# Performance work log

Hardware: AMD Instinct MI355X
Metric: run time of the kernel (lower is better)

The kernel has to match this reference:

```python
import jax, jax.numpy as jnp
import numpy as np

N = 8192        # nodes
V = 50000       # vocab = len(dict_node_names)
EMB = 256       # embedding_dim
XI = EMB // 2   # x_increased_dim = 128
DIN = EMB + XI  # 384, SelfAtt_ dim
H = 4           # n_heads
D = 128         # WGAT output_dim per head (fusion dim)
E = 131072      # edges
CHUNK = 32768   # chunk_size (E % CHUNK == 0)


def _ln(x, g, b, eps=1e-5):
    m = jnp.mean(x, axis=-1, keepdims=True)
    v = jnp.mean((x - m) ** 2, axis=-1, keepdims=True)
    return (x - m) * jax.lax.rsqrt(v + eps) * g + b


def _wgat(emb, src, dst, edge_attr, wi, bi, wj, bj, wt, bt, attn):
    # x_i = features at destination (aggregation target), x_j = source/neighbor
    x_i = emb[dst]                                   # [E, din]
    x_j = emb[src]                                   # [E, din]
    h = (x_i @ wi + bi).reshape(E, H, D) + (x_j @ wj + bj).reshape(E, H, D)
    a = jnp.einsum('ehd,hd->eh', h, attn)            # [E, H]
    a = a * edge_attr[:, None]                       # edge weights pre-softmax
    # faithful chunked softmax: normalize over edges WITHIN each chunk (dim=0 per chunk)
    a = jax.nn.softmax(a.reshape(E // CHUNK, CHUNK, H), axis=1).reshape(E, H)
    xt = (x_j @ wt + bt).reshape(E, H, D)            # [E, H, D]
    msg = jnp.einsum('ehd,eh->ed', xt, a)            # sum over heads -> [E, D]
    return jax.ops.segment_sum(msg, dst, num_segments=N)  # aggr='add'


def _emb_forward(ids, edge_index, x, edge_attr, embed,
                 qkv_w, qkv_b, proj_w, proj_b, fuse_w, fuse_b, ln1_g, ln1_b,
                 wi0, bi0, wj0, bj0, wt0, bt0, attn0, skip0_w, skip0_b,
                 wi1, bi1, wj1, bj1, wt1, bt1, attn1, skip1_w, skip1_b,
                 ln2_g, ln2_b):
    E_i = embed[ids]                                 # [N, EMB] gather
    z = jnp.concatenate([jnp.tile(x, (1, XI)), E_i], axis=-1)   # [N, DIN]
    # SelfAtt_ : full N x N attention over nodes, scale = DIN**-0.5
    qkv = z @ qkv_w + qkv_b
    q, k, v = jnp.split(qkv, 3, axis=-1)
    att = jax.nn.softmax((q @ k.T) * (DIN ** -0.5), axis=-1) @ v
    z = att @ proj_w + proj_b                        # [N, DIN]
    emb = jax.nn.silu(_ln(z @ fuse_w + fuse_b, ln1_g, ln1_b)) + E_i  # [N, EMB]
    src, dst = edge_index[0], edge_index[1]
    emb = _wgat(emb, src, dst, edge_attr, wi0, bi0, wj0, bj0, wt0, bt0, attn0)  # [N, D]
    s0 = emb @ skip0_w + skip0_b
    emb = _wgat(emb, src, dst, edge_attr, wi1, bi1, wj1, bj1, wt1, bt1, attn1)  # [N, D]
    s1 = emb @ skip1_w + skip1_b
    emb = _ln(emb + (s0 + s1) * 0.5, ln2_g, ln2_b)
    return emb


def setup_inputs() -> dict:
    key = jax.random.key(0)
    ks = jax.random.split(key, 32)

    def w(k, shape, scale=0.05):
        return jax.random.normal(k, shape, jnp.float32) * scale

    inp = {}
    inp['ids'] = jax.random.randint(ks[0], (N,), 0, V)
    inp['x'] = jax.random.normal(ks[1], (N, 1), jnp.float32)
    inp['edge_attr'] = jax.random.uniform(ks[2], (E,), jnp.float32)
    inp['edge_index'] = jax.random.randint(ks[3], (2, E), 0, N)
    inp['embed'] = w(ks[4], (V, EMB), 1.0)
    inp['qkv_w'] = w(ks[5], (DIN, 3 * DIN)); inp['qkv_b'] = jnp.zeros((3 * DIN,), jnp.float32)
    inp['proj_w'] = w(ks[6], (DIN, DIN));    inp['proj_b'] = jnp.zeros((DIN,), jnp.float32)
    inp['fuse_w'] = w(ks[7], (DIN, EMB));    inp['fuse_b'] = jnp.zeros((EMB,), jnp.float32)
    inp['ln1_g'] = jnp.ones((EMB,), jnp.float32); inp['ln1_b'] = jnp.zeros((EMB,), jnp.float32)
    # WGAT layer 0: in=EMB, out=D per head, H heads
    inp['wi0'] = w(ks[8], (EMB, H * D));  inp['bi0'] = jnp.zeros((H * D,), jnp.float32)
    inp['wj0'] = w(ks[9], (EMB, H * D));  inp['bj0'] = jnp.zeros((H * D,), jnp.float32)
    inp['wt0'] = w(ks[10], (EMB, H * D)); inp['bt0'] = jnp.zeros((H * D,), jnp.float32)
    inp['attn0'] = w(ks[11], (H, D), 0.1)
    inp['skip0_w'] = w(ks[12], (D, D));   inp['skip0_b'] = jnp.zeros((D,), jnp.float32)
    # WGAT layer 1: in=D
    inp['wi1'] = w(ks[13], (D, H * D));   inp['bi1'] = jnp.zeros((H * D,), jnp.float32)
    inp['wj1'] = w(ks[14], (D, H * D));   inp['bj1'] = jnp.zeros((H * D,), jnp.float32)
    inp['wt1'] = w(ks[15], (D, H * D));   inp['bt1'] = jnp.zeros((H * D,), jnp.float32)
    inp['attn1'] = w(ks[16], (H, D), 0.1)
    inp['skip1_w'] = w(ks[17], (D, D));   inp['skip1_b'] = jnp.zeros((D,), jnp.float32)
    inp['ln2_g'] = jnp.ones((D,), jnp.float32); inp['ln2_b'] = jnp.zeros((D,), jnp.float32)
    return inp


def reference(ids, x, edge_attr, edge_index, embed,
              qkv_w, qkv_b, proj_w, proj_b, fuse_w, fuse_b, ln1_g, ln1_b,
              wi0, bi0, wj0, bj0, wt0, bt0, attn0, skip0_w, skip0_b,
              wi1, bi1, wj1, bj1, wt1, bt1, attn1, skip1_w, skip1_b,
              ln2_g, ln2_b):
    emb = _emb_forward(ids, edge_index, x, edge_attr, embed,
                       qkv_w, qkv_b, proj_w, proj_b, fuse_w, fuse_b, ln1_g, ln1_b,
                       wi0, bi0, wj0, bj0, wt0, bt0, attn0, skip0_w, skip0_b,
                       wi1, bi1, wj1, bj1, wt1, bt1, attn1, skip1_w, skip1_b,
                       ln2_g, ln2_b)
    return (emb, embed, ids)
```

## Files before the change

### kernel.cpp

```cpp
#include <hip/hip_runtime.h>

typedef __attribute__((ext_vector_type(8))) short bfrag;
typedef __attribute__((ext_vector_type(4))) float f4;

#define MFMA(a,b,c) __builtin_amdgcn_mfma_f32_16x16x32_bf16(a,b,c,0,0,0)

__device__ __forceinline__ unsigned short f2b(float x){
  union { float f; unsigned int u; } v; v.f = x;
  unsigned int r = v.u + 0x7fffu + ((v.u >> 16) & 1u);
  return (unsigned short)(r >> 16);
}
__device__ __forceinline__ float b2f(unsigned short h){
  union { unsigned int u; float f; } v; v.u = ((unsigned int)h) << 16;
  return v.f;
}

__global__ __launch_bounds__(256) void k_prep(
    const float* __restrict__ qkv_w, const float* __restrict__ proj_w,
    const float* __restrict__ proj_b, const float* __restrict__ fuse_w,
    const float* __restrict__ fuse_b,
    const float* __restrict__ wt0,
    const float* __restrict__ wt1, const float* __restrict__ sk0w,
    const float* __restrict__ wi0, const float* __restrict__ bi0,
    const float* __restrict__ wj0, const float* __restrict__ bj0,
    const float* __restrict__ wi1, const float* __restrict__ bi1,
    const float* __restrict__ wj1, const float* __restrict__ bj1,
    const float* __restrict__ attn0, const float* __restrict__ attn1,
    const float* __restrict__ bt0, const float* __restrict__ bt1,
    const float* __restrict__ sk0b,
    const float* __restrict__ embed, const int* __restrict__ ids,
    unsigned short* __restrict__ BtQKV, unsigned short* __restrict__ BtW2,
    unsigned short* __restrict__ BtT0, unsigned short* __restrict__ BtT1,
    float* __restrict__ biasW2,
    float* __restrict__ biasT0, float* __restrict__ biasT1,
    float* __restrict__ wsum, float* __restrict__ Ei,
    float* __restrict__ out)
{
  int b = blockIdx.x, t = threadIdx.x;
  if (b < 1152) {
    int idx = b*256 + t; int k = idx/1152, n = idx - k*1152;
    BtQKV[(size_t)n*256 + k] = f2b(qkv_w[128*1152 + idx]);
  } else if (b < 1536) {
    int k = b - 1152;
    float s = 0.f;
    for (int j = 0; j < 384; ++j) s += proj_w[(size_t)k*384 + j] * fuse_w[(size_t)j*256 + t];
    BtW2[(size_t)t*384 + k] = f2b(s);
  } else if (b == 1536) {
    float s = fuse_b[t];
    for (int j = 0; j < 384; ++j) s += proj_b[j] * fuse_w[(size_t)j*256 + t];
    biasW2[t] = s;
  } else if (b < 2049) {
    int idx = (b-1537)*256 + t; int k = idx/512, n = idx - k*512;
    BtT0[(size_t)n*256 + k] = f2b(wt0[idx]);
  } else if (b < 2305) {
    int idx = (b-2049)*256 + t; int k = idx/512, n = idx - k*512;
    BtT1[(size_t)n*128 + k] = f2b(wt1[idx]);
  } else if (b < 2369) {
    int idx = (b-2305)*256 + t; int k = idx/128, n = idx - k*128;
    BtT1[(size_t)(520+n)*128 + k] = f2b(sk0w[idx]);
  } else if (b < 2373) {
    int idx = (b-2369)*256 + t;
    int h = idx >> 8, k = idx & 255;
    float s = 0.f;
    for (int d = 0; d < 128; ++d) s += wi0[(size_t)k*512 + h*128 + d] * attn0[h*128 + d];
    BtT0[(size_t)(512 + h)*256 + k] = f2b(s);
    if (idx < 4) {
      float sb = 0.f;
      for (int d = 0; d < 128; ++d) sb += bi0[idx*128 + d] * attn0[idx*128 + d];
      biasT0[512 + idx] = sb;
    }
  } else if (b < 2377) {
    int idx = (b-2373)*256 + t;
    int h = idx >> 8, k = idx & 255;
    float s = 0.f;
    for (int d = 0; d < 128; ++d) s += wj0[(size_t)k*512 + h*128 + d] * attn0[h*128 + d];
    BtT0[(size_t)(516 + h)*256 + k] = f2b(s);
    if (idx < 4) {
      float sb = 0.f;
      for (int d = 0; d < 128; ++d) sb += bj0[idx*128 + d] * attn0[idx*128 + d];
      biasT0[516 + idx] = sb;
    }
  } else if (b < 2379) {
    int idx = (b-2377)*256 + t;
    int h = idx >> 7, k = idx & 127;
    float s = 0.f;
    for (int d = 0; d < 128; ++d) s += wi1[(size_t)k*512 + h*128 + d] * attn1[h*128 + d];
    BtT1[(size_t)(512 + h)*128 + k] = f2b(s);
    if (idx < 4) {
      float sb = 0.f;
      for (int d = 0; d < 128; ++d) sb += bi1[idx*128 + d] * attn1[idx*128 + d];
      biasT1[512 + idx] = sb;
    }
  } else if (b < 2381) {
    int idx = (b-2379)*256 + t;
    int h = idx >> 7, k = idx & 127;
    float s = 0.f;
    for (int d = 0; d < 128; ++d) s += wj1[(size_t)k*512 + h*128 + d] * attn1[h*128 + d];
    BtT1[(size_t)(516 + h)*128 + k] = f2b(s);
    if (idx < 4) {
      float sb = 0.f;
      for (int d = 0; d < 128; ++d) sb += bj1[idx*128 + d] * attn1[idx*128 + d];
      biasT1[516 + idx] = sb;
    }
  } else if (b < 2383) {
    int idx = (b-2381)*256 + t; biasT0[idx] = bt0[idx];
  } else if (b < 2385) {
    int idx = (b-2383)*256 + t; biasT1[idx] = bt1[idx];
  } else if (b == 2385) {
    if (t < 128) biasT1[520 + t] = sk0b[t];
  } else if (b < 2391) {
    int n = (b-2386)*256 + t;
    if (n < 1152) {
      float s = 0.f;
      for (int k = 0; k < 128; ++k) s += qkv_w[(size_t)k*1152 + n];
      wsum[n] = s;
    }
  } else if (b < 4439) {
    int idx = (b-2391)*256 + t;
    int n = idx >> 6, c4 = idx & 63;
    reinterpret_cast<float4*>(Ei)[idx] =
        reinterpret_cast<const float4*>(embed + (size_t)ids[n]*256)[c4];
  } else {
    int i = (b-4439)*256 + t;
    if (i < 3200000)
      reinterpret_cast<float4*>(out)[262144 + i] = reinterpret_cast<const float4*>(embed)[i];
    if (i < 8192) out[13848576 + i] = (float)ids[i];
  }
}

__global__ void k_deg(const int* __restrict__ ei, int* __restrict__ deg){
  int e = blockIdx.x*256 + threadIdx.x; if (e >= 131072) return;
  atomicAdd(&deg[ei[131072 + e]], 1);
}

__global__ __launch_bounds__(1024) void k_scan(const int* __restrict__ deg,
                                               int* __restrict__ off, int* __restrict__ cursor){
  int t = threadIdx.x;
  int v[8]; int s = 0;
  #pragma unroll
  for (int i=0;i<8;++i){ v[i] = s; s += deg[t*8 + i]; }
  int lane = t & 63, w = t >> 6;
  int si = s;
  for (int o=1;o<64;o<<=1){ int u = __shfl_up(si, o); if (lane >= o) si += u; }
  __shared__ int wsum[16];
  if (lane == 63) wsum[w] = si;
  __syncthreads();
  if (t < 16) {
    int x = wsum[t];
    for (int o=1;o<16;o<<=1){ int u = __shfl_up(x, o); if (t >= o) x += u; }
    wsum[t] = x;
  }
  __syncthreads();
  int wbase = (w == 0) ? 0 : wsum[w-1];
  int base = wbase + (si - s);
  #pragma unroll
  for (int i=0;i<8;++i){ int o2 = base + v[i]; off[t*8+i] = o2; cursor[t*8+i] = o2; }
  if (t == 1023) off[8192] = wbase + si;
}

__global__ void k_fill(const int* __restrict__ ei, int* __restrict__ cursor,
                       int* __restrict__ elist){
  int e = blockIdx.x*256 + threadIdx.x; if (e >= 131072) return;
  int d = ei[131072 + e];
  int slot = atomicAdd(&cursor[d], 1);
  elist[slot] = e;
}

__global__ __launch_bounds__(256) void k_gemm(
    const float* __restrict__ A, int lda,
    const unsigned short* __restrict__ Bt, int K,
    const float* __restrict__ bias,
    float* __restrict__ C, int ldc, int mode,
    const float* __restrict__ xv, const float* __restrict__ wsum,
    unsigned short* __restrict__ qO, unsigned short* __restrict__ kO,
    unsigned short* __restrict__ vO,
    const unsigned short* __restrict__ opA, const float* __restrict__ cw,
    float* __restrict__ aux, int ncols)
{
  __shared__ unsigned short As[128*40];
  __shared__ unsigned short Bs[128*40];
  const int t = threadIdx.x;
  const int wid = t >> 6, l = t & 63;
  const int lr = l & 15, lg = l >> 4;
  const int arow0 = blockIdx.y*128, bn0 = blockIdx.x*128;
  const int wr = (wid >> 1)*64, wc = (wid & 1)*64;
  f4 zero = {0.f,0.f,0.f,0.f};
  f4 acc[4][4];
  #pragma unroll
  for (int i=0;i<4;++i)
    #pragma unroll
    for (int j=0;j<4;++j) acc[i][j] = zero;

  for (int k0 = 0; k0 < K; k0 += 32) {
    #pragma unroll
    for (int p=0;p<4;++p) {
      int row = p*32 + (t>>3);
      int c4  = (t&7)*4;
      ushort4 h4;
      if (mode == 2) {
        const float* w4 = &cw[(arow0+row)*4];
        float a0=0.f,a1=0.f,a2=0.f,a3=0.f;
        #pragma unroll
        for (int s=0;s<4;++s) {
          ushort4 u = *reinterpret_cast<const ushort4*>(
              opA + (size_t)s*3145728 + (size_t)(arow0+row)*384 + k0 + c4);
          float wv = w4[s];
          a0 += b2f(u.x)*wv; a1 += b2f(u.y)*wv; a2 += b2f(u.z)*wv; a3 += b2f(u.w)*wv;
        }
        h4.x = f2b(a0); h4.y = f2b(a1); h4.z = f2b(a2); h4.w = f2b(a3);
      } else {
        float4 v = *reinterpret_cast<const float4*>(A + (size_t)(arow0+row)*lda + k0 + c4);
        h4.x = f2b(v.x); h4.y = f2b(v.y); h4.z = f2b(v.z); h4.w = f2b(v.w);
      }
      *reinterpret_cast<ushort4*>(&As[row*40 + c4]) = h4;
    }
    #pragma unroll
    for (int p=0;p<2;++p) {
      int n  = p*64 + (t>>2);
      int c8 = (t&3)*8;
      int4 v = *reinterpret_cast<const int4*>(Bt + (size_t)(bn0+n)*K + k0 + c8);
      *reinterpret_cast<int4*>(&Bs[n*40 + c8]) = v;
    }
    __syncthreads();
    bfrag af[4], bfm[4];
    #pragma unroll
    for (int mi=0;mi<4;++mi) af[mi] = *reinterpret_cast<const bfrag*>(&As[(wr+mi*16+lr)*40 + lg*8]);
    #pragma unroll
    for (int ni=0;ni<4;++ni) bfm[ni] = *reinterpret_cast<const bfrag*>(&Bs[(wc+ni*16+lr)*40 + lg*8]);
    #pragma unroll
    for (int mi=0;mi<4;++mi)
      #pragma unroll
      for (int ni=0;ni<4;++ni)
        acc[mi][ni] = MFMA(af[mi], bfm[ni], acc[mi][ni]);
    __syncthreads();
  }
  #pragma unroll
  for (int mi=0;mi<4;++mi) {
    #pragma unroll
    for (int ni=0;ni<4;++ni) {
      int col = bn0 + wc + ni*16 + lr;
      float bv = bias[col];
      float wsv = (mode==1) ? wsum[col] : 0.f;
      #pragma unroll
      for (int i=0;i<4;++i) {
        int row = arow0 + wr + mi*16 + lg*4 + i;
        float val = acc[mi][ni][i] + bv;
        if (mode == 1) {
          val += xv[row]*wsv;
          if (col < 384) val *= 0.05103103631f;
          unsigned short hv = f2b(val);
          if (col < 384)      qO[(size_t)row*384 + col] = hv;
          else if (col < 768) kO[(size_t)row*384 + col - 384] = hv;
          else {
            int d = col - 768, j = row;
            size_t vidx = (size_t)(j >> 5)*12288 + (size_t)(d >> 4)*512
                        + (size_t)(d & 15)*32 + (size_t)((j & 31) >> 3)*8 + (j & 7);
            vO[vidx] = hv;
          }
        } else if (mode == 3) {
          if (col < 512)      qO[(size_t)row*512 + col] = f2b(val);
          else if (col < 520) C[(size_t)row*8 + col - 512] = val;
          else if (col < ncols) aux[(size_t)row*128 + col - 520] = val;
        } else {
          C[(size_t)row*ldc + col] = val;
        }
      }
    }
  }
}

__global__ __launch_bounds__(256,2) void k_flash(
    const unsigned short* __restrict__ qg,
    const unsigned short* __restrict__ kg,
    const unsigned short* __restrict__ vg,
    unsigned short* __restrict__ Opart, float* __restrict__ mpart, float* __restrict__ lpart)
{
  __shared__ unsigned short Ks[32*384];
  __shared__ unsigned short Ps[64*40];
  __shared__ float f_s[64];

  const int t = threadIdx.x;
  const int w = t >> 6, l = t & 63;
  const int lr = l & 15, lg = l >> 4;
  const int qbi = blockIdx.x >> 2, split = blockIdx.x & 3;
  const int qbase = qbi * 64;

  #define STAGE_K(JJ) do { \
    _Pragma("unroll") \
    for (int p_=0;p_<6;++p_) { \
      int idx_ = p_*256 + t; \
      int row_ = idx_ / 48, uu_ = idx_ - row_*48; \
      int ug_ = uu_ ^ (row_ & 7); \
      const unsigned short* gp_ = kg + (size_t)((JJ) + row_)*384 + ug_*8; \
      __builtin_amdgcn_global_load_lds((const __attribute__((address_space(1))) void*)gp_, \
          (__attribute__((address_space(3))) void*)&Ks[idx_*8], 16, 0, 0); \
    } } while(0)

  bfrag qf[12];
  #pragma unroll
  for (int kk=0;kk<12;++kk)
    qf[kk] = *reinterpret_cast<const bfrag*>(qg + (size_t)(qbase + w*16 + lr)*384 + kk*32 + lg*8);

  f4 zero = {0.f,0.f,0.f,0.f};
  f4 o[4][6];
  #pragma unroll
  for (int a=0;a<4;++a)
    #pragma unroll
    for (int b=0;b<6;++b) o[a][b] = zero;

  float m = -3e38f, lsum = 0.f;
  const int j0beg = split*2048, jend = j0beg + 2048;

  STAGE_K(j0beg);
  __syncthreads();

  for (int j0 = j0beg; j0 < jend; j0 += 32) {
    f4 s0 = zero, s1 = zero;
    __builtin_amdgcn_s_setprio(1);
    #pragma unroll
    for (int kk=0;kk<12;++kk) {
      int su = ((kk*4 + lg) ^ (lr & 7)) * 8;
      bfrag k0 = *reinterpret_cast<const bfrag*>(&Ks[lr*384 + su]);
      bfrag k1 = *reinterpret_cast<const bfrag*>(&Ks[(16+lr)*384 + su]);
      s0 = MFMA(k0, qf[kk], s0);
      s1 = MFMA(k1, qf[kk], s1);
    }
    __builtin_amdgcn_s_setprio(0);

    float mt = fmaxf(fmaxf(fmaxf(s0[0],s0[1]),fmaxf(s0[2],s0[3])),
                     fmaxf(fmaxf(s1[0],s1[1]),fmaxf(s1[2],s1[3])));
    mt = fmaxf(mt, __shfl_xor(mt,16));
    mt = fmaxf(mt, __shfl_xor(mt,32));
    bool grew = mt > m + 8.f;
    bool doresc = __any(grew);
    float mn = doresc ? fmaxf(m, mt) : m;
    float p0[4], p1[4];
    float sum = 0.f;
    #pragma unroll
    for (int i=0;i<4;++i) {
      p0[i] = __expf(s0[i]-mn); p1[i] = __expf(s1[i]-mn);
      sum += p0[i] + p1[i];
    }
    sum += __shfl_xor(sum,16);
    sum += __shfl_xor(sum,32);
    float f = 1.f;
    if (doresc) {
      f = __expf(m - mn);
      lsum = lsum * f + sum;
      m = mn;
    } else {
      lsum += sum;
    }

    unsigned int pk0 = (unsigned int)f2b(p0[0]) | ((unsigned int)f2b(p0[1]) << 16);
    unsigned int pk1 = (unsigned int)f2b(p0[2]) | ((unsigned int)f2b(p0[3]) << 16);
    unsigned int pk2 = (unsigned int)f2b(p1[0]) | ((unsigned int)f2b(p1[1]) << 16);
    unsigned int pk3 = (unsigned int)f2b(p1[2]) | ((unsigned int)f2b(p1[3]) << 16);
    int prow = (w*16 + lr)*40;
    *reinterpret_cast<unsigned int*>(&Ps[prow + lg*4])          = pk0;
    *reinterpret_cast<unsigned int*>(&Ps[prow + lg*4 + 2])      = pk1;
    *reinterpret_cast<unsigned int*>(&Ps[prow + 16 + lg*4])     = pk2;
    *reinterpret_cast<unsigned int*>(&Ps[prow + 16 + lg*4 + 2]) = pk3;
    if (lg == 0) f_s[w*16 + lr] = f;

    __syncthreads();

    if (j0 + 32 < jend) STAGE_K(j0 + 32);

    const int jt = j0 >> 5;
    bfrag vf[6];
    #pragma unroll
    for (int dt=0;dt<6;++dt)
      vf[dt] = *reinterpret_cast<const bfrag*>(
          vg + (size_t)jt*12288 + (size_t)(w*6 + dt)*512 + lr*32 + lg*8);

    bfrag pf[4];
    #pragma unroll
    for (int qt=0;qt<4;++qt)
      pf[qt] = *reinterpret_cast<const bfrag*>(&Ps[(qt*16+lr)*40 + lg*8]);
    #pragma unroll
    for (int qt=0;qt<4;++qt) {
      #pragma unroll
      for (int i=0;i<4;++i) {
        float frv = f_s[qt*16 + lg*4 + i];
        #pragma unroll
        for (int dt=0;dt<6;++dt) o[qt][dt][i] *= frv;
      }
    }
    __builtin_amdgcn_s_setprio(1);
    #pragma unroll
    for (int qt=0;qt<4;++qt)
      #pragma unroll
      for (int dt=0;dt<6;++dt)
        o[qt][dt] = MFMA(pf[qt], vf[dt], o[qt][dt]);
    __builtin_amdgcn_s_setprio(0);

    __syncthreads();
  }
  #undef STAGE_K

  unsigned short* Op = Opart + (size_t)split*8192*384;
  #pragma unroll
  for (int qt=0;qt<4;++qt)
    #pragma unroll
    for (int dt=0;dt<6;++dt)
      #pragma unroll
      for (int i=0;i<4;++i)
        Op[(size_t)(qbase + qt*16 + lg*4 + i)*384 + w*96 + dt*16 + lr] = f2b(o[qt][dt][i]);
  if (lg == 0) {
    mpart[split*8192 + qbase + w*16 + lr] = m;
    lpart[split*8192 + qbase + w*16 + lr] = lsum;
  }
}

__global__ void k_cw(const float* __restrict__ mp, const float* __restrict__ lp,
                     float* __restrict__ cw)
{
  int r = blockIdx.x*256 + threadIdx.x;
  float m0 = mp[r], m1 = mp[8192+r], m2 = mp[16384+r], m3 = mp[24576+r];
  float M = fmaxf(fmaxf(m0,m1), fmaxf(m2,m3));
  float w0 = __expf(m0-M), w1 = __expf(m1-M), w2 = __expf(m2-M), w3 = __expf(m3-M);
  float L = lp[r]*w0 + lp[8192+r]*w1 + lp[16384+r]*w2 + lp[24576+r]*w3;
  float inv = 1.f / L;
  float4 o4 = make_float4(w0*inv, w1*inv, w2*inv, w3*inv);
  *reinterpret_cast<float4*>(&cw[r*4]) = o4;
}

__global__ __launch_bounds__(256) void k_ln1(const float* __restrict__ pre, const float* __restrict__ Ei,
                      const float* __restrict__ g, const float* __restrict__ b,
                      float* __restrict__ out)
{
  int row = blockIdx.x, c = threadIdx.x;
  float v = pre[(size_t)row*256 + c];
  float s1 = v, s2 = v*v;
  #pragma unroll
  for (int o1=32;o1;o1>>=1){ s1 += __shfl_down(s1,o1); s2 += __shfl_down(s2,o1); }
  __shared__ float a1[4], a2[4];
  if ((c&63)==0){ a1[c>>6] = s1; a2[c>>6] = s2; }
  __syncthreads();
  float S1 = a1[0]+a1[1]+a1[2]+a1[3], S2 = a2[0]+a2[1]+a2[2]+a2[3];
  float mean = S1*(1.f/256.f), var = S2*(1.f/256.f) - mean*mean;
  float y = (v-mean)*rsqrtf(var+1e-5f)*g[c] + b[c];
  float sig = 1.f/(1.f+__expf(-y));
  out[(size_t)row*256 + c] = y*sig + Ei[(size_t)row*256 + c];
}

__global__ __launch_bounds__(256) void k_escore(const int* __restrict__ ei, const float* __restrict__ ea,
                         const float* __restrict__ SC, float* __restrict__ sc,
                         float* __restrict__ pm, float* __restrict__ ps)
{
  int e = blockIdx.x*256 + threadIdx.x;
  int s = ei[e], d = ei[131072 + e];
  float wv = ea[e];
  float4 ai = *reinterpret_cast<const float4*>(&SC[(size_t)d*8]);
  float4 aj = *reinterpret_cast<const float4*>(&SC[(size_t)s*8 + 4]);
  float4 o4 = make_float4((ai.x+aj.x)*wv, (ai.y+aj.y)*wv, (ai.z+aj.z)*wv, (ai.w+aj.w)*wv);
  *reinterpret_cast<float4*>(&sc[e*4]) = o4;

  float sv[4] = {o4.x, o4.y, o4.z, o4.w};
  __shared__ float sm_[4][4], ss_[4][4];
  int lane = threadIdx.x & 63, wvid = threadIdx.x >> 6;
  #pragma unroll
  for (int h=0; h<4; ++h) {
    float m = sv[h], s2 = 1.f;
    #pragma unroll
    for (int o1=32;o1;o1>>=1) {
      float om = __shfl_xor(m,o1), os = __shfl_xor(s2,o1);
      float M2 = fmaxf(m,om);
      s2 = s2*__expf(m-M2) + os*__expf(om-M2);
      m = M2;
    }
    if (lane==0){ sm_[wvid][h]=m; ss_[wvid][h]=s2; }
  }
  __syncthreads();
  if (threadIdx.x < 4) {
    int h = threadIdx.x;
    float M = sm_[0][h], S = ss_[0][h];
    #pragma unroll
    for (int i=1;i<4;++i){
      float M2 = fmaxf(M, sm_[i][h]);
      S = S*__expf(M-M2) + ss_[i][h]*__expf(sm_[i][h]-M2);
      M = M2;
    }
    pm[blockIdx.x*4+h] = M; ps[blockIdx.x*4+h] = S;
  }
}

__global__ __launch_bounds__(128) void k_cfin(const float* __restrict__ pm, const float* __restrict__ ps,
                                              float* __restrict__ mx, float* __restrict__ sm)
{
  int ch = blockIdx.x;
  int c = ch >> 2, h = ch & 3;
  int t = threadIdx.x;
  float M = pm[(c*128 + t)*4 + h], S = ps[(c*128 + t)*4 + h];
  int lane = t & 63;
  #pragma unroll
  for (int o1=32;o1;o1>>=1){
    float om = __shfl_xor(M,o1), os = __shfl_xor(S,o1);
    float M2 = fmaxf(M,om);
    S = S*__expf(M-M2) + os*__expf(om-M2);
    M = M2;
  }
  __shared__ float am[2], as[2];
  if (lane==0){ am[t>>6]=M; as[t>>6]=S; }
  __syncthreads();
  if (t==0){
    float M2 = fmaxf(am[0],am[1]);
    float Sf = as[0]*__expf(am[0]-M2) + as[1]*__expf(am[1]-M2);
    mx[ch]=M2; sm[ch]=Sf;
  }
}

__global__ void k_pnorm(float* __restrict__ sc, const float* __restrict__ mx,
                        const float* __restrict__ sm)
{
  int i = blockIdx.x*256 + threadIdx.x;
  int e = i >> 2, h = i & 3;
  int ch = (e >> 15)*4 + h;
  sc[i] = __expf(sc[i] - mx[ch]) / sm[ch];
}

__global__ __launch_bounds__(128) void k_aggr(const int* __restrict__ off,
                      const int* __restrict__ elist, const int* __restrict__ ei,
                      const float* __restrict__ sc,
                      const unsigned short* __restrict__ Tb, float* __restrict__ g)
{
  int n = blockIdx.x, d = threadIdx.x;
  int qb = off[n], qe = off[n+1];
  float acc = 0.f;
  for (int q = qb; q < qe; ++q) {
    int e = elist[q];
    int s = ei[e];
    float4 p = *reinterpret_cast<const float4*>(&sc[e*4]);
    const unsigned short* Tr = Tb + (size_t)s*512;
    acc += p.x*b2f(Tr[d]) + p.y*b2f(Tr[128+d]) + p.z*b2f(Tr[256+d]) + p.w*b2f(Tr[384+d]);
  }
  g[(size_t)n*128 + d] = acc;
}

__global__ __launch_bounds__(128) void k_final(const float* __restrict__ g1, const float* __restrict__ aux,
                       const float* __restrict__ sw, const float* __restrict__ sb,
                       const float* __restrict__ lg2, const float* __restrict__ lb2,
                       float* __restrict__ out)
{
  int row = blockIdx.x, c = threadIdx.x;
  __shared__ float gr[128];
  float gv = g1[(size_t)row*128 + c];
  gr[c] = gv; __syncthreads();
  float s1 = sb[c];
  #pragma unroll 8
  for (int k=0;k<128;++k) s1 += gr[k]*sw[k*128 + c];
  float s0 = aux[(size_t)row*128 + c];
  float v = gv + 0.5f*(s0 + s1);
  float m1 = v, m2 = v*v;
  #pragma unroll
  for (int o1=32;o1;o1>>=1){ m1 += __shfl_down(m1,o1); m2 += __shfl_down(m2,o1); }
  __shared__ float a1[2], a2[2];
  if ((c&63)==0){ a1[c>>6]=m1; a2[c>>6]=m2; }
  __syncthreads();
  float S1 = a1[0]+a1[1], S2 = a2[0]+a2[1];
  float mean = S1*(1.f/128.f), var = S2*(1.f/128.f) - mean*mean;
  out[(size_t)row*128 + c] = (v-mean)*rsqrtf(var+1e-5f)*lg2[c] + lb2[c];
}

extern "C" void kernel_launch(void* const* d_in, const int* in_sizes, int n_in,
                              void* d_out, int out_size, void* d_ws, size_t ws_size,
                              hipStream_t stream)
{
  const int*   ids    = (const int*)  d_in[0];
  const float* x      = (const float*)d_in[1];
  const float* ea     = (const float*)d_in[2];
  const int*   eidx   = (const int*)  d_in[3];
  const float* embed  = (const float*)d_in[4];
  const float* qkv_w  = (const float*)d_in[5];
  const float* qkv_b  = (const float*)d_in[6];
  const float* proj_w = (const float*)d_in[7];
  const float* proj_b = (const float*)d_in[8];
  const float* fuse_w = (const float*)d_in[9];
  const float* fuse_b = (const float*)d_in[10];
  const float* ln1_g  = (const float*)d_in[11];
  const float* ln1_b  = (const float*)d_in[12];
  const float* wi0 = (const float*)d_in[13]; const float* bi0 = (const float*)d_in[14];
  const float* wj0 = (const float*)d_in[15]; const float* bj0 = (const float*)d_in[16];
  const float* wt0 = (const float*)d_in[17]; const float* bt0 = (const float*)d_in[18];
  const float* attn0 = (const float*)d_in[19];
  const float* sk0w = (const float*)d_in[20]; const float* sk0b = (const float*)d_in[21];
  const float* wi1 = (const float*)d_in[22]; const float* bi1 = (const float*)d_in[23];
  const float* wj1 = (const float*)d_in[24]; const float* bj1 = (const float*)d_in[25];
  const float* wt1 = (const float*)d_in[26]; const float* bt1 = (const float*)d_in[27];
  const float* attn1 = (const float*)d_in[28];
  const float* sk1w = (const float*)d_in[29]; const float* sk1b = (const float*)d_in[30];
  const float* ln2_g = (const float*)d_in[31]; const float* ln2_b = (const float*)d_in[32];

  char* ws = (char*)d_ws;
  const size_t MBy = (size_t)1 << 20;

  unsigned short* BtQKV  = (unsigned short*)(ws + 0);
  unsigned short* BtW2   = (unsigned short*)(ws + 589824);
  float* biasW2 = (float*)(ws + 884736);
  unsigned short* BtT0   = (unsigned short*)(ws + 1081344);
  unsigned short* BtT1   = (unsigned short*)(ws + 1409024);
  float* biasT0 = (float*)(ws + 1605632);
  float* biasT1 = (float*)(ws + 1608192);
  float* wsum   = (float*)(ws + 1611264);
  float* mxb    = (float*)(ws + 1615872);
  float* smb    = (float*)(ws + 1615936);
  int* deg    = (int*)(ws + 1703936);
  int* cursor = (int*)(ws + 1736704);
  int* off    = (int*)(ws + 1769472);
  float* cw   = (float*)(ws + 1806336);
  float* pm   = (float*)(ws + 1937408);
  float* ps   = (float*)(ws + 1945600);

  float* Ei   = (float*)(ws + 2*MBy);
  unsigned short* qb = (unsigned short*)(ws + 10*MBy);
  unsigned short* kb = (unsigned short*)(ws + 17*MBy);
  unsigned short* vb = (unsigned short*)(ws + 24*MBy);
  unsigned short* Opart = (unsigned short*)(ws + 31*MBy);
  float* mpart = (float*)(ws + 55*MBy);
  float* lpart = (float*)(ws + 55*MBy + 131072);
  float* pre  = (float*)(ws + 10*MBy);
  float* emb0 = (float*)(ws + 31*MBy);
  unsigned short* TCb0 = (unsigned short*)(ws + 39*MBy);
  float* SCb0 = (float*)(ws + 47*MBy);
  float* SCb1 = (float*)(ws + 47*MBy + 262144);
  float* AUX  = (float*)(ws + 47*MBy + 524288);
  float* sc0  = (float*)(ws + 52*MBy);
  float* sc1  = (float*)(ws + 54*MBy);
  unsigned short* TCb1 = (unsigned short*)(ws + 18*MBy);
  float* g0   = (float*)(ws + 2*MBy);
  float* g1   = (float*)(ws + 6*MBy);
  int* elist  = (int*)(ws + 62*MBy);

  float* out = (float*)d_out;

  hipMemsetAsync(ws, 0, 2*MBy, stream);

  k_prep<<<16939, 256, 0, stream>>>(qkv_w, proj_w, proj_b, fuse_w, fuse_b,
                                    wt0, wt1, sk0w,
                                    wi0, bi0, wj0, bj0, wi1, bi1, wj1, bj1,
                                    attn0, attn1, bt0, bt1, sk0b, embed, ids,
                                    BtQKV, BtW2, BtT0, BtT1,
                                    biasW2, biasT0, biasT1, wsum, Ei, out);
  k_deg<<<512, 256, 0, stream>>>(eidx, deg);
  k_scan<<<1, 1024, 0, stream>>>(deg, off, cursor);
  k_fill<<<512, 256, 0, stream>>>(eidx, cursor, elist);

  k_gemm<<<dim3(9,64), 256, 0, stream>>>(Ei, 256, BtQKV, 256, qkv_b, nullptr, 0, 1,
                                         x, wsum, qb, kb, vb, nullptr, nullptr,
                                         nullptr, 0);
  k_flash<<<512, 256, 0, stream>>>(qb, kb, vb, Opart, mpart, lpart);
  k_cw<<<32, 256, 0, stream>>>(mpart, lpart, cw);

  k_gemm<<<dim3(2,64), 256, 0, stream>>>(nullptr, 0, BtW2, 384, biasW2, pre, 256, 2,
                                         nullptr, nullptr, nullptr, nullptr, nullptr,
                                         Opart, cw, nullptr, 0);
  k_ln1<<<8192, 256, 0, stream>>>(pre, Ei, ln1_g, ln1_b, emb0);

  k_gemm<<<dim3(5,64), 256, 0, stream>>>(emb0, 256, BtT0, 256, biasT0, SCb0, 0, 3,
                                         nullptr, nullptr, TCb0, nullptr, nullptr,
                                         nullptr, nullptr, AUX, 520);
  k_escore<<<512, 256, 0, stream>>>(eidx, ea, SCb0, sc0, pm, ps);
  k_cfin<<<16, 128, 0, stream>>>(pm, ps, mxb, smb);
  k_pnorm<<<2048, 256, 0, stream>>>(sc0, mxb, smb);
  k_aggr<<<8192, 128, 0, stream>>>(off, elist, eidx, sc0, TCb0, g0);

  k_gemm<<<dim3(6,64), 256, 0, stream>>>(g0, 128, BtT1, 128, biasT1, SCb1, 0, 3,
                                         nullptr, nullptr, TCb1, nullptr, nullptr,
                                         nullptr, nullptr, AUX, 648);
  k_escore<<<512, 256, 0, stream>>>(eidx, ea, SCb1, sc1, pm, ps);
  k_cfin<<<16, 128, 0, stream>>>(pm, ps, mxb, smb);
  k_pnorm<<<2048, 256, 0, stream>>>(sc1, mxb, smb);
  k_aggr<<<8192, 128, 0, stream>>>(off, elist, eidx, sc1, TCb1, g1);

  k_final<<<8192, 128, 0, stream>>>(g1, AUX, sk1w, sk1b, ln2_g, ln2_b, out);
}
```

Before: 425.1 us.

## Pre-tile K in MFMA layout for direct global loads; fuse softmax normalize into aggregation

The QKV GEMM now writes K in a tiled layout that matches the MFMA fragment order. The flash kernel can then load K fragments straight from global memory (through L2) rather than staging them into LDS. The P and rescale buffers are double-buffered, which drops the trailing barrier in each iteration, and sched_barriers are added. Separately, the per-chunk softmax normalization kernel is removed and its exp/divide is folded into the aggregation loop. This saves two launches and a pass over the score array, but the exp is recomputed for every feature thread.

```diff
diff --git a/kernel.cpp b/kernel.cpp
--- a/kernel.cpp
+++ b/kernel.cpp
@@ -250,8 +250,13 @@
           if (col < 384) val *= 0.05103103631f;
           unsigned short hv = f2b(val);
           if (col < 384)      qO[(size_t)row*384 + col] = hv;
-          else if (col < 768) kO[(size_t)row*384 + col - 384] = hv;
-          else {
+          else if (col < 768) {
+            int c = col - 384, j = row;
+            size_t kidx = (size_t)(j >> 5)*12288 + (size_t)((j >> 4) & 1)*6144
+                        + (size_t)(c >> 5)*512 + (size_t)(j & 15)*32
+                        + (size_t)((c >> 3) & 3)*8 + (c & 7);
+            kO[kidx] = hv;
+          } else {
             int d = col - 768, j = row;
             size_t vidx = (size_t)(j >> 5)*12288 + (size_t)(d >> 4)*512
                         + (size_t)(d & 15)*32 + (size_t)((j & 31) >> 3)*8 + (j & 7);
@@ -275,9 +280,8 @@
     const unsigned short* __restrict__ vg,
     unsigned short* __restrict__ Opart, float* __restrict__ mpart, float* __restrict__ lpart)
 {
-  __shared__ unsigned short Ks[32*384];
-  __shared__ unsigned short Ps[64*40];
-  __shared__ float f_s[64];
+  __shared__ unsigned short Ps[2][64*40];
+  __shared__ float f_s[2][64];
 
   const int t = threadIdx.x;
   const int w = t >> 6, l = t & 63;
@@ -285,17 +289,6 @@
   const int qbi = blockIdx.x >> 2, split = blockIdx.x & 3;
   const int qbase = qbi * 64;
 
-  #define STAGE_K(JJ) do { \
-    _Pragma("unroll") \
-    for (int p_=0;p_<6;++p_) { \
-      int idx_ = p_*256 + t; \
-      int row_ = idx_ / 48, uu_ = idx_ - row_*48; \
-      int ug_ = uu_ ^ (row_ & 7); \
-      const unsigned short* gp_ = kg + (size_t)((JJ) + row_)*384 + ug_*8; \
-      __builtin_amdgcn_global_load_lds((const __attribute__((address_space(1))) void*)gp_, \
-          (__attribute__((address_space(3))) void*)&Ks[idx_*8], 16, 0, 0); \
-    } } while(0)
-
   bfrag qf[12];
   #pragma unroll
   for (int kk=0;kk<12;++kk)
@@ -311,19 +304,20 @@
   float m = -3e38f, lsum = 0.f;
   const int j0beg = split*2048, jend = j0beg + 2048;
 
-  STAGE_K(j0beg);
-  __syncthreads();
-
   for (int j0 = j0beg; j0 < jend; j0 += 32) {
+    const int jt = j0 >> 5;
+    const int buf = jt & 1;
+
+    const unsigned short* kbase = kg + (size_t)jt*12288 + lr*32 + lg*8;
     f4 s0 = zero, s1 = zero;
     __builtin_amdgcn_s_setprio(1);
     #pragma unroll
     for (int kk=0;kk<12;++kk) {
-      int su = ((kk*4 + lg) ^ (lr & 7)) * 8;
-      bfrag k0 = *reinterpret_cast<const bfrag*>(&Ks[lr*384 + su]);
-      bfrag k1 = *reinterpret_cast<const bfrag*>(&Ks[(16+lr)*384 + su]);
+      bfrag k0 = *reinterpret_cast<const bfrag*>(kbase + kk*512);
+      bfrag k1 = *reinterpret_cast<const bfrag*>(kbase + 6144 + kk*512);
       s0 = MFMA(k0, qf[kk], s0);
       s1 = MFMA(k1, qf[kk], s1);
+      if ((kk & 3) == 3) __builtin_amdgcn_sched_barrier(0);
     }
     __builtin_amdgcn_s_setprio(0);
 
@@ -357,17 +351,14 @@
     unsigned int pk2 = (unsigned int)f2b(p1[0]) | ((unsigned int)f2b(p1[1]) << 16);
     unsigned int pk3 = (unsigned int)f2b(p1[2]) | ((unsigned int)f2b(p1[3]) << 16);
     int prow = (w*16 + lr)*40;
-    *reinterpret_cast<unsigned int*>(&Ps[prow + lg*4])          = pk0;
-    *reinterpret_cast<unsigned int*>(&Ps[prow + lg*4 + 2])      = pk1;
-    *reinterpret_cast<unsigned int*>(&Ps[prow + 16 + lg*4])     = pk2;
-    *reinterpret_cast<unsigned int*>(&Ps[prow + 16 + lg*4 + 2]) = pk3;
-    if (lg == 0) f_s[w*16 + lr] = f;
+    *reinterpret_cast<unsigned int*>(&Ps[buf][prow + lg*4])          = pk0;
+    *reinterpret_cast<unsigned int*>(&Ps[buf][prow + lg*4 + 2])      = pk1;
+    *reinterpret_cast<unsigned int*>(&Ps[buf][prow + 16 + lg*4])     = pk2;
+    *reinterpret_cast<unsigned int*>(&Ps[buf][prow + 16 + lg*4 + 2]) = pk3;
+    if (lg == 0) f_s[buf][w*16 + lr] = f;
 
     __syncthreads();
 
-    if (j0 + 32 < jend) STAGE_K(j0 + 32);
-
-    const int jt = j0 >> 5;
     bfrag vf[6];
     #pragma unroll
     for (int dt=0;dt<6;++dt)
@@ -377,12 +368,12 @@
     bfrag pf[4];
     #pragma unroll
     for (int qt=0;qt<4;++qt)
-      pf[qt] = *reinterpret_cast<const bfrag*>(&Ps[(qt*16+lr)*40 + lg*8]);
+      pf[qt] = *reinterpret_cast<const bfrag*>(&Ps[buf][(qt*16+lr)*40 + lg*8]);
     #pragma unroll
     for (int qt=0;qt<4;++qt) {
       #pragma unroll
       for (int i=0;i<4;++i) {
-        float frv = f_s[qt*16 + lg*4 + i];
+        float frv = f_s[buf][qt*16 + lg*4 + i];
         #pragma unroll
         for (int dt=0;dt<6;++dt) o[qt][dt][i] *= frv;
       }
@@ -394,10 +385,8 @@
       for (int dt=0;dt<6;++dt)
         o[qt][dt] = MFMA(pf[qt], vf[dt], o[qt][dt]);
     __builtin_amdgcn_s_setprio(0);
-
-    __syncthreads();
-  }
-  #undef STAGE_K
+    __builtin_amdgcn_sched_barrier(0);
+  }
 
   unsigned short* Op = Opart + (size_t)split*8192*384;
   #pragma unroll
@@ -511,18 +500,10 @@
   }
 }
 
-__global__ void k_pnorm(float* __restrict__ sc, const float* __restrict__ mx,
-                        const float* __restrict__ sm)
-{
-  int i = blockIdx.x*256 + threadIdx.x;
-  int e = i >> 2, h = i & 3;
-  int ch = (e >> 15)*4 + h;
-  sc[i] = __expf(sc[i] - mx[ch]) / sm[ch];
-}
-
 __global__ __launch_bounds__(128) void k_aggr(const int* __restrict__ off,
                       const int* __restrict__ elist, const int* __restrict__ ei,
                       const float* __restrict__ sc,
+                      const float* __restrict__ mx, const float* __restrict__ sm,
                       const unsigned short* __restrict__ Tb, float* __restrict__ g)
 {
   int n = blockIdx.x, d = threadIdx.x;
@@ -531,9 +512,14 @@
   for (int q = qb; q < qe; ++q) {
     int e = elist[q];
     int s = ei[e];
-    float4 p = *reinterpret_cast<const float4*>(&sc[e*4]);
+    int ch = (e >> 15) * 4;
+    float4 sv = *reinterpret_cast<const float4*>(&sc[e*4]);
+    float px = __expf(sv.x - mx[ch+0]) / sm[ch+0];
+    float py = __expf(sv.y - mx[ch+1]) / sm[ch+1];
+    float pz = __expf(sv.z - mx[ch+2]) / sm[ch+2];
+    float pw = __expf(sv.w - mx[ch+3]) / sm[ch+3];
     const unsigned short* Tr = Tb + (size_t)s*512;
-    acc += p.x*b2f(Tr[d]) + p.y*b2f(Tr[128+d]) + p.z*b2f(Tr[256+d]) + p.w*b2f(Tr[384+d]);
+    acc += px*b2f(Tr[d]) + py*b2f(Tr[128+d]) + pz*b2f(Tr[256+d]) + pw*b2f(Tr[384+d]);
   }
   g[(size_t)n*128 + d] = acc;
 }
@@ -662,16 +648,14 @@
                                          nullptr, nullptr, AUX, 520);
   k_escore<<<512, 256, 0, stream>>>(eidx, ea, SCb0, sc0, pm, ps);
   k_cfin<<<16, 128, 0, stream>>>(pm, ps, mxb, smb);
-  k_pnorm<<<2048, 256, 0, stream>>>(sc0, mxb, smb);
-  k_aggr<<<8192, 128, 0, stream>>>(off, elist, eidx, sc0, TCb0, g0);
+  k_aggr<<<8192, 128, 0, stream>>>(off, elist, eidx, sc0, mxb, smb, TCb0, g0);
 
   k_gemm<<<dim3(6,64), 256, 0, stream>>>(g0, 128, BtT1, 128, biasT1, SCb1, 0, 3,
                                          nullptr, nullptr, TCb1, nullptr, nullptr,
                                          nullptr, nullptr, AUX, 648);
   k_escore<<<512, 256, 0, stream>>>(eidx, ea, SCb1, sc1, pm, ps);
   k_cfin<<<16, 128, 0, stream>>>(pm, ps, mxb, smb);
-  k_pnorm<<<2048, 256, 0, stream>>>(sc1, mxb, smb);
-  k_aggr<<<8192, 128, 0, stream>>>(off, elist, eidx, sc1, TCb1, g1);
+  k_aggr<<<8192, 128, 0, stream>>>(off, elist, eidx, sc1, mxb, smb, TCb1, g1);
 
   k_final<<<8192, 128, 0, stream>>>(g1, AUX, sk1w, sk1b, ln2_g, ln2_b, out);
 }
```

Result: slower. 622.2 us (+46.4%).
